# Kernel tuning notes

Hardware: AMD Instinct MI355X
Metric: run time of the kernel (lower is better)

## Reference

```python
import jax, jax.numpy as jnp
import numpy as np

ALPHA = 0.2          # LeakyReLU negative slope
NEG_INF = -9e15      # mask value used by the torch module


def setup_inputs() -> dict:
    key = jax.random.key(0)
    k1, k2, k3, k4 = jax.random.split(key, 4)
    N, F_IN, F_OUT = 8192, 128, 128
    h = jax.random.normal(k1, (N, F_IN), dtype=jnp.float32)
    adj = jax.random.randint(k2, (N, N), 0, 2, dtype=jnp.int32)
    # xavier_uniform(gain=1.414) approximated with scaled normal init
    W = jax.random.normal(k3, (F_IN, F_OUT), dtype=jnp.float32) * (1.414 / np.sqrt(F_IN))
    a = jax.random.normal(k4, (2 * F_OUT, 1), dtype=jnp.float32) * (1.414 / np.sqrt(2 * F_OUT))
    return {"h": h, "adj": adj, "W": W, "a": a}


def reference(h, adj, W, a):
    # Wh: [N, F]
    Wh = h @ W
    F_out = W.shape[1]
    # e[i,j] = LeakyReLU( [Wh_i || Wh_j] . a ) = LeakyReLU( Wh_i.a1 + Wh_j.a2 )
    e_src = Wh @ a[:F_out, 0]   # [N]
    e_dst = Wh @ a[F_out:, 0]   # [N]
    e = jax.nn.leaky_relu(e_src[:, None] + e_dst[None, :], negative_slope=ALPHA)  # [N, N]
    attention = jax.nn.softmax(jnp.where(adj > 0, e, NEG_INF), axis=1)
    # dropout is identity in eval mode
    h_prime = attention @ Wh    # [N, F]
    return h_prime
```

## Files before the change

kernel.cpp:

```cpp
#include <hip/hip_runtime.h>
#include <hip/hip_bf16.h>


#define NN 8192
#define FF 128

typedef __bf16 bf16x8 __attribute__((ext_vector_type(8)));
typedef float floatx4 __attribute__((ext_vector_type(4)));

__device__ __forceinline__ unsigned short f2b(float f) {
    unsigned int u = __float_as_uint(f);
    return (unsigned short)((u + 0x7FFFu + ((u >> 16) & 1u)) >> 16);
}

__global__ __launch_bounds__(128) void k0_uv(const float* __restrict__ W,
                                             const float* __restrict__ a,
                                             float* __restrict__ u,
                                             float* __restrict__ v) {
    int k = blockIdx.x, t = threadIdx.x;
    float wv = W[k * FF + t];
    float p1 = wv * a[t];
    float p2 = wv * a[FF + t];
    for (int off = 32; off; off >>= 1) {
        p1 += __shfl_down(p1, off);
        p2 += __shfl_down(p2, off);
    }
    __shared__ float r[4];
    if ((t & 63) == 0) { r[(t >> 6) * 2] = p1; r[(t >> 6) * 2 + 1] = p2; }
    __syncthreads();
    if (t == 0) { u[k] = r[0] + r[2]; v[k] = r[1] + r[3]; }
}

__global__ __launch_bounds__(256) void k1_wh(const float* __restrict__ h,
                                             const float* __restrict__ W,
                                             const float* __restrict__ u,
                                             const float* __restrict__ v,
                                             unsigned short* __restrict__ WhT,
                                             float* __restrict__ e_src,
                                             float* __restrict__ e_dst) {
    __shared__ float hL[32 * 132];
    __shared__ float wL[128 * 132];
    __shared__ float uL[128], vL[128];
    __shared__ unsigned short tL[128 * 40];

    int t = threadIdx.x;
    int i0 = blockIdx.x * 32;

    {
        int row = t >> 3, c = (t & 7) * 16;
        const float4* s = (const float4*)&h[(i0 + row) * FF + c];
        float4* d = (float4*)&hL[row * 132 + c];
        #pragma unroll
        for (int j = 0; j < 4; j++) d[j] = s[j];
    }
    {
        int row = t >> 1, c = (t & 1) * 64;
        const float4* s = (const float4*)&W[row * FF + c];
        float4* d = (float4*)&wL[row * 132 + c];
        #pragma unroll
        for (int j = 0; j < 16; j++) d[j] = s[j];
    }
    if (t < 128) { uL[t] = u[t]; vL[t] = v[t]; }
    __syncthreads();

    int r0 = (t & 7) * 4;
    int c0 = (t >> 3) * 4;
    float acc[4][4] = {};
    for (int k0 = 0; k0 < 128; k0 += 4) {
        float4 hr[4], wr[4];
        #pragma unroll
        for (int i = 0; i < 4; i++) hr[i] = *(const float4*)&hL[(r0 + i) * 132 + k0];
        #pragma unroll
        for (int i = 0; i < 4; i++) wr[i] = *(const float4*)&wL[(k0 + i) * 132 + c0];
        #pragma unroll
        for (int kj = 0; kj < 4; kj++) {
            const float* hv0 = (const float*)&hr[0];
            #pragma unroll
            for (int ri = 0; ri < 4; ri++) {
                float hvv = ((const float*)&hr[ri])[kj];
                const float* wvv = (const float*)&wr[kj];
                #pragma unroll
                for (int cj = 0; cj < 4; cj++) acc[ri][cj] = fmaf(hvv, wvv[cj], acc[ri][cj]);
            }
            (void)hv0;
        }
    }
    #pragma unroll
    for (int ri = 0; ri < 4; ri++)
        #pragma unroll
        for (int cj = 0; cj < 4; cj++)
            tL[(c0 + cj) * 40 + r0 + ri] = f2b(acc[ri][cj]);
    __syncthreads();

    if (t < 64) {
        int row = t & 31;
        const float* sv = (t < 32) ? uL : vL;
        float s = 0.f;
        for (int k = 0; k < 128; k += 4) {
            float4 h4 = *(const float4*)&hL[row * 132 + k];
            float4 s4 = *(const float4*)&sv[k];
            s = fmaf(h4.x, s4.x, s); s = fmaf(h4.y, s4.y, s);
            s = fmaf(h4.z, s4.z, s); s = fmaf(h4.w, s4.w, s);
        }
        (t < 32 ? e_src : e_dst)[i0 + row] = s;
    }
    {
        int f = t & 127, half = t >> 7;
        const uint4* s = (const uint4*)&tL[f * 40 + half * 16];
        uint4* d = (uint4*)&WhT[f * NN + i0 + half * 16];
        d[0] = s[0]; d[1] = s[1];
    }
}

__device__ __forceinline__ float mask_w(int a, float x) {
    float l = fmaxf(x, 0.2f * x);
    return a > 0 ? __expf(l) : 0.f;
}

__global__ __launch_bounds__(512) void k2_gat(const int* __restrict__ adj,
                                              const unsigned short* __restrict__ WhT,
                                              const float* __restrict__ e_src,
                                              const float* __restrict__ e_dst,
                                              float* __restrict__ out) {
    __shared__ unsigned short wt[32 * 72];
    __shared__ float esL[32];
    __shared__ float dpart[32 * 16];
    __shared__ float denomL[32];

    int t = threadIdx.x;
    int i0 = blockIdx.x * 32;
    if (t < 32) esL[t] = e_src[i0 + t];

    int ii = t & 31;
    int q  = t >> 5;
    int jj0 = q * 4;
    int lane = t & 63, wave = t >> 6;
    int mrow = lane & 15, quad = lane >> 4;
    int n0 = wave * 16;

    const unsigned short* Bbase = WhT + (size_t)(n0 + mrow) * NN + quad * 8;
    const int* Abase = adj + (size_t)(i0 + ii) * NN + jj0;

    floatx4 acc0 = {0.f, 0.f, 0.f, 0.f};
    floatx4 acc1 = {0.f, 0.f, 0.f, 0.f};
    float dsum = 0.f;
    __syncthreads();
    float es_i = esL[ii];

    for (int j0 = 0; j0 < NN; j0 += 64) {
        int4 av = *(const int4*)(Abase + j0);
        float4 ed = *(const float4*)&e_dst[j0 + jj0];
        bf16x8 b0 = *(const bf16x8*)(Bbase + j0);
        bf16x8 b1 = *(const bf16x8*)(Bbase + j0 + 32);

        float w0 = mask_w(av.x, es_i + ed.x);
        float w1 = mask_w(av.y, es_i + ed.y);
        float w2 = mask_w(av.z, es_i + ed.z);
        float w3 = mask_w(av.w, es_i + ed.w);
        dsum += (w0 + w1) + (w2 + w3);
        ushort4 wp = make_ushort4(f2b(w0), f2b(w1), f2b(w2), f2b(w3));

        __syncthreads();
        *(ushort4*)&wt[ii * 72 + jj0] = wp;
        __syncthreads();

        bf16x8 a00 = *(const bf16x8*)&wt[mrow * 72 + quad * 8];
        bf16x8 a10 = *(const bf16x8*)&wt[(16 + mrow) * 72 + quad * 8];
        bf16x8 a01 = *(const bf16x8*)&wt[mrow * 72 + 32 + quad * 8];
        bf16x8 a11 = *(const bf16x8*)&wt[(16 + mrow) * 72 + 32 + quad * 8];

        acc0 = __builtin_amdgcn_mfma_f32_16x16x32_bf16(a00, b0, acc0, 0, 0, 0);
        acc1 = __builtin_amdgcn_mfma_f32_16x16x32_bf16(a10, b0, acc1, 0, 0, 0);
        acc0 = __builtin_amdgcn_mfma_f32_16x16x32_bf16(a01, b1, acc0, 0, 0, 0);
        acc1 = __builtin_amdgcn_mfma_f32_16x16x32_bf16(a11, b1, acc1, 0, 0, 0);
    }

    dpart[ii * 16 + q] = dsum;
    __syncthreads();
    if (t < 32) {
        float s = 0.f;
        #pragma unroll
        for (int k = 0; k < 16; k++) s += dpart[t * 16 + k];
        denomL[t] = 1.0f / s;
    }
    __syncthreads();

    #pragma unroll
    for (int r = 0; r < 4; r++) {
        int row0 = quad * 4 + r;
        out[(i0 + row0) * FF + n0 + mrow] = acc0[r] * denomL[row0];
        int row1 = 16 + row0;
        out[(i0 + row1) * FF + n0 + mrow] = acc1[r] * denomL[row1];
    }
}

extern "C" void kernel_launch(void* const* d_in, const int* in_sizes, int n_in,
                              void* d_out, int out_size, void* d_ws, size_t ws_size,
                              hipStream_t stream) {
    const float* h   = (const float*)d_in[0];
    const int*   adj = (const int*)d_in[1];
    const float* W   = (const float*)d_in[2];
    const float* a   = (const float*)d_in[3];
    float* out = (float*)d_out;

    char* ws = (char*)d_ws;
    unsigned short* WhT = (unsigned short*)ws;
    float* u     = (float*)(ws + 2097152);
    float* v     = u + 128;
    float* e_src = v + 128;
    float* e_dst = e_src + NN;

    k0_uv<<<dim3(128), dim3(128), 0, stream>>>(W, a, u, v);
    k1_wh<<<dim3(256), dim3(256), 0, stream>>>(h, W, u, v, WhT, e_src, e_dst);
    k2_gat<<<dim3(256), dim3(512), 0, stream>>>(adj, WhT, e_src, e_dst, out);
}
```

Baseline: 492.6 us.

## Split GAT reduction over column segments with atomics, double-buffered LDS and swizzle

Splits the N-long column reduction of the attention kernel into four segments so the grid grows from 256 to 1024 blocks, and combines the partial numerators and denominators with float atomics followed by a separate normalization kernel. The main loop is software-pipelined: global loads for the next tile are issued before the MFMAs on the current tile, and the LDS weight tile is double-buffered so only one barrier per iteration remains. The LDS layout is XOR-swizzled to avoid bank conflicts. The cost is two memsets, an extra kernel launch, atomic traffic on the output, and nondeterministic summation order.

New measurement: 419.3 us. 1.17x faster.

```diff
diff --git a/kernel.cpp b/kernel.cpp
--- a/kernel.cpp
+++ b/kernel.cpp
@@ -4,6 +4,9 @@
 
 #define NN 8192
 #define FF 128
+#define SEG 4
+#define JSEG (NN / SEG)
+#define ITERS (JSEG / 64)
 
 typedef __bf16 bf16x8 __attribute__((ext_vector_type(8)));
 typedef float floatx4 __attribute__((ext_vector_type(4)));
@@ -74,7 +77,6 @@
         for (int i = 0; i < 4; i++) wr[i] = *(const float4*)&wL[(k0 + i) * 132 + c0];
         #pragma unroll
         for (int kj = 0; kj < 4; kj++) {
-            const float* hv0 = (const float*)&hr[0];
             #pragma unroll
             for (int ri = 0; ri < 4; ri++) {
                 float hvv = ((const float*)&hr[ri])[kj];
@@ -82,7 +84,6 @@
                 #pragma unroll
                 for (int cj = 0; cj < 4; cj++) acc[ri][cj] = fmaf(hvv, wvv[cj], acc[ri][cj]);
             }
-            (void)hv0;
         }
     }
     #pragma unroll
@@ -117,29 +118,39 @@
     return a > 0 ? __expf(l) : 0.f;
 }
 
-__global__ __launch_bounds__(512) void k2_gat(const int* __restrict__ adj,
-                                              const unsigned short* __restrict__ WhT,
-                                              const float* __restrict__ e_src,
-                                              const float* __restrict__ e_dst,
-                                              float* __restrict__ out) {
-    __shared__ unsigned short wt[32 * 72];
+__global__ __launch_bounds__(512, 4) void k2_gat(const int* __restrict__ adj,
+                                                 const unsigned short* __restrict__ WhT,
+                                                 const float* __restrict__ e_src,
+                                                 const float* __restrict__ e_dst,
+                                                 float* __restrict__ num,
+                                                 float* __restrict__ den) {
+    __shared__ unsigned short wt[2][32 * 64];
     __shared__ float esL[32];
-    __shared__ float dpart[32 * 16];
-    __shared__ float denomL[32];
+    __shared__ float dpart[32 * 17];
 
     int t = threadIdx.x;
-    int i0 = blockIdx.x * 32;
+    int bx = blockIdx.x;
+    int g = bx >> 2, seg = bx & 3;
+    int i0 = g * 32;
+    int jbase = seg * JSEG;
+
     if (t < 32) esL[t] = e_src[i0 + t];
 
     int ii = t & 31;
     int q  = t >> 5;
-    int jj0 = q * 4;
     int lane = t & 63, wave = t >> 6;
     int mrow = lane & 15, quad = lane >> 4;
     int n0 = wave * 16;
 
-    const unsigned short* Bbase = WhT + (size_t)(n0 + mrow) * NN + quad * 8;
-    const int* Abase = adj + (size_t)(i0 + ii) * NN + jj0;
+    const unsigned short* Bb = WhT + (size_t)(n0 + mrow) * NN + jbase + quad * 8;
+    const int*   Ab = adj + (size_t)(i0 + ii) * NN + jbase + q * 4;
+    const float* Eb = e_dst + jbase + q * 4;
+
+    int waddr = ii * 64 + (((q >> 1) ^ (ii & 7)) << 3) + ((q & 1) << 2);
+    int ra00 = mrow * 64 + ((quad ^ (mrow & 7)) << 3);
+    int ra01 = mrow * 64 + (((4 + quad) ^ (mrow & 7)) << 3);
+    int ra10 = (16 + mrow) * 64 + ((quad ^ (mrow & 7)) << 3);
+    int ra11 = (16 + mrow) * 64 + (((4 + quad) ^ (mrow & 7)) << 3);
 
     floatx4 acc0 = {0.f, 0.f, 0.f, 0.f};
     floatx4 acc1 = {0.f, 0.f, 0.f, 0.f};
@@ -147,51 +158,85 @@
     __syncthreads();
     float es_i = esL[ii];
 
-    for (int j0 = 0; j0 < NN; j0 += 64) {
-        int4 av = *(const int4*)(Abase + j0);
-        float4 ed = *(const float4*)&e_dst[j0 + jj0];
-        bf16x8 b0 = *(const bf16x8*)(Bbase + j0);
-        bf16x8 b1 = *(const bf16x8*)(Bbase + j0 + 32);
-
+    int4   av = *(const int4*)Ab;
+    float4 ed = *(const float4*)Eb;
+    bf16x8 b0 = *(const bf16x8*)Bb;
+    bf16x8 b1 = *(const bf16x8*)(Bb + 32);
+    {
         float w0 = mask_w(av.x, es_i + ed.x);
         float w1 = mask_w(av.y, es_i + ed.y);
         float w2 = mask_w(av.z, es_i + ed.z);
         float w3 = mask_w(av.w, es_i + ed.w);
         dsum += (w0 + w1) + (w2 + w3);
-        ushort4 wp = make_ushort4(f2b(w0), f2b(w1), f2b(w2), f2b(w3));
-
-        __syncthreads();
-        *(ushort4*)&wt[ii * 72 + jj0] = wp;
-        __syncthreads();
-
-        bf16x8 a00 = *(const bf16x8*)&wt[mrow * 72 + quad * 8];
-        bf16x8 a10 = *(const bf16x8*)&wt[(16 + mrow) * 72 + quad * 8];
-        bf16x8 a01 = *(const bf16x8*)&wt[mrow * 72 + 32 + quad * 8];
-        bf16x8 a11 = *(const bf16x8*)&wt[(16 + mrow) * 72 + 32 + quad * 8];
-
+        *(ushort4*)&wt[0][waddr] = make_ushort4(f2b(w0), f2b(w1), f2b(w2), f2b(w3));
+    }
+    __syncthreads();
+
+    for (int k = 0; k < ITERS - 1; k++) {
+        int joff = (k + 1) * 64;
+        int4   av2 = *(const int4*)(Ab + joff);
+        float4 ed2 = *(const float4*)(Eb + joff);
+        bf16x8 nb0 = *(const bf16x8*)(Bb + joff);
+        bf16x8 nb1 = *(const bf16x8*)(Bb + joff + 32);
+
+        const unsigned short* buf = wt[k & 1];
+        bf16x8 a00 = *(const bf16x8*)&buf[ra00];
+        bf16x8 a10 = *(const bf16x8*)&buf[ra10];
+        bf16x8 a01 = *(const bf16x8*)&buf[ra01];
+        bf16x8 a11 = *(const bf16x8*)&buf[ra11];
         acc0 = __builtin_amdgcn_mfma_f32_16x16x32_bf16(a00, b0, acc0, 0, 0, 0);
         acc1 = __builtin_amdgcn_mfma_f32_16x16x32_bf16(a10, b0, acc1, 0, 0, 0);
         acc0 = __builtin_amdgcn_mfma_f32_16x16x32_bf16(a01, b1, acc0, 0, 0, 0);
         acc1 = __builtin_amdgcn_mfma_f32_16x16x32_bf16(a11, b1, acc1, 0, 0, 0);
-    }
-
-    dpart[ii * 16 + q] = dsum;
+
+        float w0 = mask_w(av2.x, es_i + ed2.x);
+        float w1 = mask_w(av2.y, es_i + ed2.y);
+        float w2 = mask_w(av2.z, es_i + ed2.z);
+        float w3 = mask_w(av2.w, es_i + ed2.w);
+        dsum += (w0 + w1) + (w2 + w3);
+        *(ushort4*)&wt[(k + 1) & 1][waddr] = make_ushort4(f2b(w0), f2b(w1), f2b(w2), f2b(w3));
+        b0 = nb0; b1 = nb1;
+        __syncthreads();
+    }
+    {
+        const unsigned short* buf = wt[(ITERS - 1) & 1];
+        bf16x8 a00 = *(const bf16x8*)&buf[ra00];
+        bf16x8 a10 = *(const bf16x8*)&buf[ra10];
+        bf16x8 a01 = *(const bf16x8*)&buf[ra01];
+        bf16x8 a11 = *(const bf16x8*)&buf[ra11];
+        acc0 = __builtin_amdgcn_mfma_f32_16x16x32_bf16(a00, b0, acc0, 0, 0, 0);
+        acc1 = __builtin_amdgcn_mfma_f32_16x16x32_bf16(a10, b0, acc1, 0, 0, 0);
+        acc0 = __builtin_amdgcn_mfma_f32_16x16x32_bf16(a01, b1, acc0, 0, 0, 0);
+        acc1 = __builtin_amdgcn_mfma_f32_16x16x32_bf16(a11, b1, acc1, 0, 0, 0);
+    }
+
+    dpart[ii * 17 + q] = dsum;
     __syncthreads();
     if (t < 32) {
         float s = 0.f;
         #pragma unroll
-        for (int k = 0; k < 16; k++) s += dpart[t * 16 + k];
-        denomL[t] = 1.0f / s;
-    }
-    __syncthreads();
+        for (int k = 0; k < 16; k++) s += dpart[t * 17 + k];
+        atomicAdd(&den[i0 + t], s);
+    }
 
     #pragma unroll
     for (int r = 0; r < 4; r++) {
         int row0 = quad * 4 + r;
-        out[(i0 + row0) * FF + n0 + mrow] = acc0[r] * denomL[row0];
-        int row1 = 16 + row0;
-        out[(i0 + row1) * FF + n0 + mrow] = acc1[r] * denomL[row1];
-    }
+        atomicAdd(&num[(size_t)(i0 + row0) * FF + n0 + mrow], acc0[r]);
+        atomicAdd(&num[(size_t)(i0 + 16 + row0) * FF + n0 + mrow], acc1[r]);
+    }
+}
+
+__global__ __launch_bounds__(256) void k3_scale(float* __restrict__ out,
+                                                const float* __restrict__ den) {
+    int idx = blockIdx.x * 256 + threadIdx.x;
+    int i = idx >> 5;
+    int c = (idx & 31) << 2;
+    float r = 1.0f / den[i];
+    float4* p = (float4*)&out[(size_t)i * FF + c];
+    float4 v = *p;
+    v.x *= r; v.y *= r; v.z *= r; v.w *= r;
+    *p = v;
 }
 
 extern "C" void kernel_launch(void* const* d_in, const int* in_sizes, int n_in,
@@ -209,8 +254,13 @@
     float* v     = u + 128;
     float* e_src = v + 128;
     float* e_dst = e_src + NN;
+    float* den   = e_dst + NN;
+
+    hipMemsetAsync(out, 0, (size_t)NN * FF * sizeof(float), stream);
+    hipMemsetAsync(den, 0, (size_t)NN * sizeof(float), stream);
 
     k0_uv<<<dim3(128), dim3(128), 0, stream>>>(W, a, u, v);
     k1_wh<<<dim3(256), dim3(256), 0, stream>>>(h, W, u, v, WhT, e_src, e_dst);
-    k2_gat<<<dim3(256), dim3(512), 0, stream>>>(adj, WhT, e_src, e_dst, out);
-}
+    k2_gat<<<dim3(256 * SEG), dim3(512), 0, stream>>>(adj, WhT, e_src, e_dst, out, den);
+    k3_scale<<<dim3(NN * FF / 4 / 256), dim3(256), 0, stream>>>(out, den);
+}
```

## Split GAT aggregation over key segments with larger row tiles and merge pass

Applied to the files above, without the earlier changes.

Restructures the attention-aggregation kernel so each block handles 128 rows over one eighth of the key dimension, with 8 waves tiling a 128x128 output and reusing each WhT fragment across more rows. It adds a double-buffered, XOR-swizzled LDS tile for the bf16 attention weights, prefetches the next adjacency chunk, and drops to one barrier per step. Partial numerators and denominators go to workspace and a new merge kernel sums and normalizes them. This raises parallelism (512 blocks instead of 256) and cuts redundant WhT reads, at the cost of a 32MB partial-sum round trip and an extra launch.

Result: faster. 425.4 us (-13.6%).

```diff
diff --git a/kernel.cpp b/kernel.cpp
--- a/kernel.cpp
+++ b/kernel.cpp
@@ -4,6 +4,10 @@
 
 #define NN 8192
 #define FF 128
+#define SEGS 8
+#define KSEG (NN / SEGS)
+#define KC 64
+#define NCH (KSEG / KC)
 
 typedef __bf16 bf16x8 __attribute__((ext_vector_type(8)));
 typedef float floatx4 __attribute__((ext_vector_type(4)));
@@ -11,6 +15,9 @@
 __device__ __forceinline__ unsigned short f2b(float f) {
     unsigned int u = __float_as_uint(f);
     return (unsigned short)((u + 0x7FFFu + ((u >> 16) & 1u)) >> 16);
+}
+__device__ __forceinline__ unsigned int pk2(float a, float b) {
+    return (unsigned int)f2b(a) | ((unsigned int)f2b(b) << 16);
 }
 
 __global__ __launch_bounds__(128) void k0_uv(const float* __restrict__ W,
@@ -74,7 +81,6 @@
         for (int i = 0; i < 4; i++) wr[i] = *(const float4*)&wL[(k0 + i) * 132 + c0];
         #pragma unroll
         for (int kj = 0; kj < 4; kj++) {
-            const float* hv0 = (const float*)&hr[0];
             #pragma unroll
             for (int ri = 0; ri < 4; ri++) {
                 float hvv = ((const float*)&hr[ri])[kj];
@@ -82,7 +88,6 @@
                 #pragma unroll
                 for (int cj = 0; cj < 4; cj++) acc[ri][cj] = fmaf(hvv, wvv[cj], acc[ri][cj]);
             }
-            (void)hv0;
         }
     }
     #pragma unroll
@@ -117,81 +122,155 @@
     return a > 0 ? __expf(l) : 0.f;
 }
 
-__global__ __launch_bounds__(512) void k2_gat(const int* __restrict__ adj,
-                                              const unsigned short* __restrict__ WhT,
-                                              const float* __restrict__ e_src,
-                                              const float* __restrict__ e_dst,
-                                              float* __restrict__ out) {
-    __shared__ unsigned short wt[32 * 72];
-    __shared__ float esL[32];
-    __shared__ float dpart[32 * 16];
-    __shared__ float denomL[32];
+__global__ __launch_bounds__(512, 4) void k2_gat(const int* __restrict__ adj,
+                                                 const unsigned short* __restrict__ WhT,
+                                                 const float* __restrict__ e_src,
+                                                 const float* __restrict__ e_dst,
+                                                 float* __restrict__ num_ws,
+                                                 float* __restrict__ den_ws) {
+    __shared__ unsigned short Pt[2][128 * 64];
 
     int t = threadIdx.x;
-    int i0 = blockIdx.x * 32;
-    if (t < 32) esL[t] = e_src[i0 + t];
-
-    int ii = t & 31;
-    int q  = t >> 5;
-    int jj0 = q * 4;
+    int bx = blockIdx.x;
+    int ib = bx >> 3, seg = bx & 7;
+    int i0 = ib * 128;
+    int jb = seg * KSEG;
+
+    int pr = t >> 2;
+    int pc = (t & 3) * 16;
+    int r7 = pr & 7;
+    int g0 = (t & 3) * 2;
+    float es = e_src[i0 + pr];
+    const int*   Ab = adj + (size_t)(i0 + pr) * NN + jb + pc;
+    const float* Eb = e_dst + jb + pc;
+    int wlo = pr * 64 + (((g0 + 0) ^ r7) << 3);
+    int whi = pr * 64 + (((g0 + 1) ^ r7) << 3);
+
     int lane = t & 63, wave = t >> 6;
+    int mg = wave & 3, ng = wave >> 2;
     int mrow = lane & 15, quad = lane >> 4;
-    int n0 = wave * 16;
-
-    const unsigned short* Bbase = WhT + (size_t)(n0 + mrow) * NN + quad * 8;
-    const int* Abase = adj + (size_t)(i0 + ii) * NN + jj0;
-
-    floatx4 acc0 = {0.f, 0.f, 0.f, 0.f};
-    floatx4 acc1 = {0.f, 0.f, 0.f, 0.f};
+
+    const unsigned short* Bp[4];
+    #pragma unroll
+    for (int bn = 0; bn < 4; bn++)
+        Bp[bn] = WhT + (size_t)(ng * 64 + bn * 16 + mrow) * NN + jb + quad * 8;
+
+    int arow[2];
+    arow[0] = mg * 32 + mrow;
+    arow[1] = mg * 32 + 16 + mrow;
+    int aoff[2][2];
+    #pragma unroll
+    for (int a = 0; a < 2; a++)
+        #pragma unroll
+        for (int ks = 0; ks < 2; ks++)
+            aoff[a][ks] = arow[a] * 64 + (((ks * 4 + quad) ^ (arow[a] & 7)) << 3);
+
+    floatx4 acc[2][4] = {};
     float dsum = 0.f;
-    __syncthreads();
-    float es_i = esL[ii];
-
-    for (int j0 = 0; j0 < NN; j0 += 64) {
-        int4 av = *(const int4*)(Abase + j0);
-        float4 ed = *(const float4*)&e_dst[j0 + jj0];
-        bf16x8 b0 = *(const bf16x8*)(Bbase + j0);
-        bf16x8 b1 = *(const bf16x8*)(Bbase + j0 + 32);
-
-        float w0 = mask_w(av.x, es_i + ed.x);
-        float w1 = mask_w(av.y, es_i + ed.y);
-        float w2 = mask_w(av.z, es_i + ed.z);
-        float w3 = mask_w(av.w, es_i + ed.w);
-        dsum += (w0 + w1) + (w2 + w3);
-        ushort4 wp = make_ushort4(f2b(w0), f2b(w1), f2b(w2), f2b(w3));
+
+    int4 av[4];
+    #pragma unroll
+    for (int j = 0; j < 4; j++) av[j] = *(const int4*)(Ab + 4 * j);
+
+    for (int ch = 0; ch < NCH; ch++) {
+        unsigned short* buf = Pt[ch & 1];
+        float4 ev0 = *(const float4*)(Eb + ch * KC);
+        float4 ev1 = *(const float4*)(Eb + ch * KC + 4);
+        float4 ev2 = *(const float4*)(Eb + ch * KC + 8);
+        float4 ev3 = *(const float4*)(Eb + ch * KC + 12);
+        float w[16];
+        w[0]  = mask_w(av[0].x, es + ev0.x);
+        w[1]  = mask_w(av[0].y, es + ev0.y);
+        w[2]  = mask_w(av[0].z, es + ev0.z);
+        w[3]  = mask_w(av[0].w, es + ev0.w);
+        w[4]  = mask_w(av[1].x, es + ev1.x);
+        w[5]  = mask_w(av[1].y, es + ev1.y);
+        w[6]  = mask_w(av[1].z, es + ev1.z);
+        w[7]  = mask_w(av[1].w, es + ev1.w);
+        w[8]  = mask_w(av[2].x, es + ev2.x);
+        w[9]  = mask_w(av[2].y, es + ev2.y);
+        w[10] = mask_w(av[2].z, es + ev2.z);
+        w[11] = mask_w(av[2].w, es + ev2.w);
+        w[12] = mask_w(av[3].x, es + ev3.x);
+        w[13] = mask_w(av[3].y, es + ev3.y);
+        w[14] = mask_w(av[3].z, es + ev3.z);
+        w[15] = mask_w(av[3].w, es + ev3.w);
+        #pragma unroll
+        for (int j = 0; j < 16; j++) dsum += w[j];
+        uint4 lo = make_uint4(pk2(w[0], w[1]), pk2(w[2], w[3]),
+                              pk2(w[4], w[5]), pk2(w[6], w[7]));
+        uint4 hi = make_uint4(pk2(w[8], w[9]), pk2(w[10], w[11]),
+                              pk2(w[12], w[13]), pk2(w[14], w[15]));
+        *(uint4*)&buf[wlo] = lo;
+        *(uint4*)&buf[whi] = hi;
+
+        int nxt = (ch + 1 < NCH) ? (ch + 1) * KC : 0;
+        #pragma unroll
+        for (int j = 0; j < 4; j++) av[j] = *(const int4*)(Ab + nxt + 4 * j);
+
+        bf16x8 b0[4];
+        #pragma unroll
+        for (int bn = 0; bn < 4; bn++) b0[bn] = *(const bf16x8*)(Bp[bn] + ch * KC);
 
         __syncthreads();
-        *(ushort4*)&wt[ii * 72 + jj0] = wp;
-        __syncthreads();
-
-        bf16x8 a00 = *(const bf16x8*)&wt[mrow * 72 + quad * 8];
-        bf16x8 a10 = *(const bf16x8*)&wt[(16 + mrow) * 72 + quad * 8];
-        bf16x8 a01 = *(const bf16x8*)&wt[mrow * 72 + 32 + quad * 8];
-        bf16x8 a11 = *(const bf16x8*)&wt[(16 + mrow) * 72 + 32 + quad * 8];
-
-        acc0 = __builtin_amdgcn_mfma_f32_16x16x32_bf16(a00, b0, acc0, 0, 0, 0);
-        acc1 = __builtin_amdgcn_mfma_f32_16x16x32_bf16(a10, b0, acc1, 0, 0, 0);
-        acc0 = __builtin_amdgcn_mfma_f32_16x16x32_bf16(a01, b1, acc0, 0, 0, 0);
-        acc1 = __builtin_amdgcn_mfma_f32_16x16x32_bf16(a11, b1, acc1, 0, 0, 0);
-    }
-
-    dpart[ii * 16 + q] = dsum;
-    __syncthreads();
-    if (t < 32) {
-        float s = 0.f;
-        #pragma unroll
-        for (int k = 0; k < 16; k++) s += dpart[t * 16 + k];
-        denomL[t] = 1.0f / s;
-    }
-    __syncthreads();
-
-    #pragma unroll
-    for (int r = 0; r < 4; r++) {
-        int row0 = quad * 4 + r;
-        out[(i0 + row0) * FF + n0 + mrow] = acc0[r] * denomL[row0];
-        int row1 = 16 + row0;
-        out[(i0 + row1) * FF + n0 + mrow] = acc1[r] * denomL[row1];
-    }
+
+        const unsigned short* rbuf = Pt[ch & 1];
+        bf16x8 A0[2], A1[2];
+        #pragma unroll
+        for (int a = 0; a < 2; a++) A0[a] = *(const bf16x8*)&rbuf[aoff[a][0]];
+        #pragma unroll
+        for (int a = 0; a < 2; a++) A1[a] = *(const bf16x8*)&rbuf[aoff[a][1]];
+
+        bf16x8 b1[4];
+        #pragma unroll
+        for (int bn = 0; bn < 4; bn++) b1[bn] = *(const bf16x8*)(Bp[bn] + ch * KC + 32);
+
+        #pragma unroll
+        for (int a = 0; a < 2; a++)
+            #pragma unroll
+            for (int bn = 0; bn < 4; bn++)
+                acc[a][bn] = __builtin_amdgcn_mfma_f32_16x16x32_bf16(A0[a], b0[bn], acc[a][bn], 0, 0, 0);
+        #pragma unroll
+        for (int a = 0; a < 2; a++)
+            #pragma unroll
+            for (int bn = 0; bn < 4; bn++)
+                acc[a][bn] = __builtin_amdgcn_mfma_f32_16x16x32_bf16(A1[a], b1[bn], acc[a][bn], 0, 0, 0);
+    }
+
+    dsum += __shfl_xor(dsum, 1);
+    dsum += __shfl_xor(dsum, 2);
+    if ((t & 3) == 0) den_ws[seg * NN + i0 + pr] = dsum;
+
+    float* np = num_ws + (size_t)seg * NN * FF;
+    #pragma unroll
+    for (int a = 0; a < 2; a++)
+        #pragma unroll
+        for (int bn = 0; bn < 4; bn++)
+            #pragma unroll
+            for (int r = 0; r < 4; r++) {
+                int row = mg * 32 + a * 16 + quad * 4 + r;
+                int col = ng * 64 + bn * 16 + mrow;
+                np[(size_t)(i0 + row) * FF + col] = acc[a][bn][r];
+            }
+}
+
+__global__ __launch_bounds__(256) void k3_merge(const float* __restrict__ num_ws,
+                                                const float* __restrict__ den_ws,
+                                                float* __restrict__ out) {
+    int idx = blockIdx.x * 256 + threadIdx.x;
+    int i = idx >> 5;
+    int c = (idx & 31) << 2;
+    float4 s = make_float4(0.f, 0.f, 0.f, 0.f);
+    float d = 0.f;
+    #pragma unroll
+    for (int sg = 0; sg < SEGS; sg++) {
+        float4 vv = *(const float4*)&num_ws[(size_t)sg * NN * FF + (size_t)i * FF + c];
+        s.x += vv.x; s.y += vv.y; s.z += vv.z; s.w += vv.w;
+        d += den_ws[sg * NN + i];
+    }
+    float r = 1.0f / d;
+    s.x *= r; s.y *= r; s.z *= r; s.w *= r;
+    *(float4*)&out[(size_t)i * FF + c] = s;
 }
 
 extern "C" void kernel_launch(void* const* d_in, const int* in_sizes, int n_in,
@@ -207,10 +286,13 @@
     unsigned short* WhT = (unsigned short*)ws;
     float* u     = (float*)(ws + 2097152);
     float* v     = u + 128;
-    float* e_src = v + 128;
+    float* e_src = (float*)(ws + 2097152 + 1024);
     float* e_dst = e_src + NN;
+    float* num_ws = (float*)(ws + 4194304);
+    float* den_ws = (float*)(ws + 4194304 + 33554432);
 
     k0_uv<<<dim3(128), dim3(128), 0, stream>>>(W, a, u, v);
     k1_wh<<<dim3(256), dim3(256), 0, stream>>>(h, W, u, v, WhT, e_src, e_dst);
-    k2_gat<<<dim3(256), dim3(512), 0, stream>>>(adj, WhT, e_src, e_dst, out);
-}
+    k2_gat<<<dim3((NN / 128) * SEGS), dim3(512), 0, stream>>>(adj, WhT, e_src, e_dst, num_ws, den_ws);
+    k3_merge<<<dim3(NN * FF / 4 / 256), dim3(256), 0, stream>>>(num_ws, den_ws, out);
+}
```

## Split GAT aggregation over column segments with register-resident attention weights and merge pass

Applied to the files above, without the earlier changes.

The attention-aggregation kernel now gives each block 128 rows and one of 8 column segments, producing partial numerators and denominators that a new merge kernel sums and normalises. Each lane computes its own bf16 attention weights directly in MFMA A-operand layout, which removes the shared-memory round trip and the two barriers per iteration, and it prefetches the next adj and e_dst chunk. Each wave covers all 128 output features with 8 accumulators, so the WhT B-operand is reused across 16 rows instead of being refetched by many narrow blocks. In exchange it writes and rereads a 32 MB partial-sum workspace and adds an extra launch.

New measurement: 483.2 us. About the same (-1.9%).

```diff
diff --git a/kernel.cpp b/kernel.cpp
--- a/kernel.cpp
+++ b/kernel.cpp
@@ -4,6 +4,9 @@
 
 #define NN 8192
 #define FF 128
+#define SEGS 8
+#define JSEG (NN / SEGS)
+#define NK (JSEG / 32)
 
 typedef __bf16 bf16x8 __attribute__((ext_vector_type(8)));
 typedef float floatx4 __attribute__((ext_vector_type(4)));
@@ -11,6 +14,9 @@
 __device__ __forceinline__ unsigned short f2b(float f) {
     unsigned int u = __float_as_uint(f);
     return (unsigned short)((u + 0x7FFFu + ((u >> 16) & 1u)) >> 16);
+}
+__device__ __forceinline__ unsigned int pk2(float a, float b) {
+    return (unsigned int)f2b(a) | ((unsigned int)f2b(b) << 16);
 }
 
 __global__ __launch_bounds__(128) void k0_uv(const float* __restrict__ W,
@@ -74,7 +80,6 @@
         for (int i = 0; i < 4; i++) wr[i] = *(const float4*)&wL[(k0 + i) * 132 + c0];
         #pragma unroll
         for (int kj = 0; kj < 4; kj++) {
-            const float* hv0 = (const float*)&hr[0];
             #pragma unroll
             for (int ri = 0; ri < 4; ri++) {
                 float hvv = ((const float*)&hr[ri])[kj];
@@ -82,7 +87,6 @@
                 #pragma unroll
                 for (int cj = 0; cj < 4; cj++) acc[ri][cj] = fmaf(hvv, wvv[cj], acc[ri][cj]);
             }
-            (void)hv0;
         }
     }
     #pragma unroll
@@ -117,81 +121,106 @@
     return a > 0 ? __expf(l) : 0.f;
 }
 
-__global__ __launch_bounds__(512) void k2_gat(const int* __restrict__ adj,
-                                              const unsigned short* __restrict__ WhT,
-                                              const float* __restrict__ e_src,
-                                              const float* __restrict__ e_dst,
-                                              float* __restrict__ out) {
-    __shared__ unsigned short wt[32 * 72];
-    __shared__ float esL[32];
-    __shared__ float dpart[32 * 16];
-    __shared__ float denomL[32];
-
+__global__ __launch_bounds__(512, 4) void k2_gat(const int* __restrict__ adj,
+                                                 const unsigned short* __restrict__ WhT,
+                                                 const float* __restrict__ e_src,
+                                                 const float* __restrict__ e_dst,
+                                                 float* __restrict__ num_ws,
+                                                 float* __restrict__ den_ws) {
     int t = threadIdx.x;
-    int i0 = blockIdx.x * 32;
-    if (t < 32) esL[t] = e_src[i0 + t];
-
-    int ii = t & 31;
-    int q  = t >> 5;
-    int jj0 = q * 4;
+    int bx = blockIdx.x;
+    int it = bx >> 3, seg = bx & 7;
+    int i0 = it * 128;
+    int jb = seg * JSEG;
+
     int lane = t & 63, wave = t >> 6;
     int mrow = lane & 15, quad = lane >> 4;
-    int n0 = wave * 16;
-
-    const unsigned short* Bbase = WhT + (size_t)(n0 + mrow) * NN + quad * 8;
-    const int* Abase = adj + (size_t)(i0 + ii) * NN + jj0;
-
-    floatx4 acc0 = {0.f, 0.f, 0.f, 0.f};
-    floatx4 acc1 = {0.f, 0.f, 0.f, 0.f};
+    int irow = i0 + wave * 16 + mrow;
+
+    float es = e_src[irow];
+    const int*   Ap = adj + (size_t)irow * NN + jb + quad * 8;
+    const float* Ep = e_dst + jb + quad * 8;
+
+    const unsigned short* Bp[8];
+    #pragma unroll
+    for (int bn = 0; bn < 8; bn++)
+        Bp[bn] = WhT + (size_t)(bn * 16 + mrow) * NN + jb + quad * 8;
+
+    floatx4 acc[8] = {};
     float dsum = 0.f;
-    __syncthreads();
-    float es_i = esL[ii];
-
-    for (int j0 = 0; j0 < NN; j0 += 64) {
-        int4 av = *(const int4*)(Abase + j0);
-        float4 ed = *(const float4*)&e_dst[j0 + jj0];
-        bf16x8 b0 = *(const bf16x8*)(Bbase + j0);
-        bf16x8 b1 = *(const bf16x8*)(Bbase + j0 + 32);
-
-        float w0 = mask_w(av.x, es_i + ed.x);
-        float w1 = mask_w(av.y, es_i + ed.y);
-        float w2 = mask_w(av.z, es_i + ed.z);
-        float w3 = mask_w(av.w, es_i + ed.w);
-        dsum += (w0 + w1) + (w2 + w3);
-        ushort4 wp = make_ushort4(f2b(w0), f2b(w1), f2b(w2), f2b(w3));
-
-        __syncthreads();
-        *(ushort4*)&wt[ii * 72 + jj0] = wp;
-        __syncthreads();
-
-        bf16x8 a00 = *(const bf16x8*)&wt[mrow * 72 + quad * 8];
-        bf16x8 a10 = *(const bf16x8*)&wt[(16 + mrow) * 72 + quad * 8];
-        bf16x8 a01 = *(const bf16x8*)&wt[mrow * 72 + 32 + quad * 8];
-        bf16x8 a11 = *(const bf16x8*)&wt[(16 + mrow) * 72 + 32 + quad * 8];
-
-        acc0 = __builtin_amdgcn_mfma_f32_16x16x32_bf16(a00, b0, acc0, 0, 0, 0);
-        acc1 = __builtin_amdgcn_mfma_f32_16x16x32_bf16(a10, b0, acc1, 0, 0, 0);
-        acc0 = __builtin_amdgcn_mfma_f32_16x16x32_bf16(a01, b1, acc0, 0, 0, 0);
-        acc1 = __builtin_amdgcn_mfma_f32_16x16x32_bf16(a11, b1, acc1, 0, 0, 0);
-    }
-
-    dpart[ii * 16 + q] = dsum;
-    __syncthreads();
-    if (t < 32) {
-        float s = 0.f;
-        #pragma unroll
-        for (int k = 0; k < 16; k++) s += dpart[t * 16 + k];
-        denomL[t] = 1.0f / s;
-    }
-    __syncthreads();
-
-    #pragma unroll
-    for (int r = 0; r < 4; r++) {
-        int row0 = quad * 4 + r;
-        out[(i0 + row0) * FF + n0 + mrow] = acc0[r] * denomL[row0];
-        int row1 = 16 + row0;
-        out[(i0 + row1) * FF + n0 + mrow] = acc1[r] * denomL[row1];
-    }
+
+    int4   a0 = *(const int4*)Ap;
+    int4   a1 = *(const int4*)(Ap + 4);
+    float4 e0 = *(const float4*)Ep;
+    float4 e1 = *(const float4*)(Ep + 4);
+
+    for (int ks = 0; ks < NK; ks++) {
+        bf16x8 B[8];
+        #pragma unroll
+        for (int bn = 0; bn < 8; bn++)
+            B[bn] = *(const bf16x8*)(Bp[bn] + ks * 32);
+
+        int nxt = (ks + 1 < NK ? ks + 1 : ks) * 32;
+        int4   na0 = *(const int4*)(Ap + nxt);
+        int4   na1 = *(const int4*)(Ap + nxt + 4);
+        float4 ne0 = *(const float4*)(Ep + nxt);
+        float4 ne1 = *(const float4*)(Ep + nxt + 4);
+
+        float w0 = mask_w(a0.x, es + e0.x);
+        float w1 = mask_w(a0.y, es + e0.y);
+        float w2 = mask_w(a0.z, es + e0.z);
+        float w3 = mask_w(a0.w, es + e0.w);
+        float w4 = mask_w(a1.x, es + e1.x);
+        float w5 = mask_w(a1.y, es + e1.y);
+        float w6 = mask_w(a1.z, es + e1.z);
+        float w7 = mask_w(a1.w, es + e1.w);
+        dsum += ((w0 + w1) + (w2 + w3)) + ((w4 + w5) + (w6 + w7));
+
+        union { unsigned int u[4]; bf16x8 v; } af;
+        af.u[0] = pk2(w0, w1);
+        af.u[1] = pk2(w2, w3);
+        af.u[2] = pk2(w4, w5);
+        af.u[3] = pk2(w6, w7);
+        bf16x8 A = af.v;
+
+        #pragma unroll
+        for (int bn = 0; bn < 8; bn++)
+            acc[bn] = __builtin_amdgcn_mfma_f32_16x16x32_bf16(A, B[bn], acc[bn], 0, 0, 0);
+
+        a0 = na0; a1 = na1; e0 = ne0; e1 = ne1;
+    }
+
+    dsum += __shfl_xor(dsum, 16);
+    dsum += __shfl_xor(dsum, 32);
+    if (quad == 0) den_ws[seg * NN + irow] = dsum;
+
+    float* np = num_ws + (size_t)seg * NN * FF;
+    #pragma unroll
+    for (int bn = 0; bn < 8; bn++)
+        #pragma unroll
+        for (int r = 0; r < 4; r++) {
+            int row = i0 + wave * 16 + quad * 4 + r;
+            np[(size_t)row * FF + bn * 16 + mrow] = acc[bn][r];
+        }
+}
+
+__global__ __launch_bounds__(256) void k3_merge(const float* __restrict__ num_ws,
+                                                const float* __restrict__ den_ws,
+                                                float* __restrict__ out) {
+    int idx = blockIdx.x * 256 + threadIdx.x;
+    int i = idx >> 5;
+    int c = (idx & 31) << 2;
+    float4 s = make_float4(0.f, 0.f, 0.f, 0.f);
+    float d = 0.f;
+    #pragma unroll
+    for (int sg = 0; sg < SEGS; sg++) {
+        float4 vv = *(const float4*)&num_ws[(size_t)sg * NN * FF + (size_t)i * FF + c];
+        s.x += vv.x; s.y += vv.y; s.z += vv.z; s.w += vv.w;
+        d += den_ws[sg * NN + i];
+    }
+    float r = 1.0f / d;
+    s.x *= r; s.y *= r; s.z *= r; s.w *= r;
+    *(float4*)&out[(size_t)i * FF + c] = s;
 }
 
 extern "C" void kernel_launch(void* const* d_in, const int* in_sizes, int n_in,
@@ -207,10 +236,13 @@
     unsigned short* WhT = (unsigned short*)ws;
     float* u     = (float*)(ws + 2097152);
     float* v     = u + 128;
-    float* e_src = v + 128;
+    float* e_src = (float*)(ws + 2097152 + 1024);
     float* e_dst = e_src + NN;
+    float* num_ws = (float*)(ws + 4194304);
+    float* den_ws = (float*)(ws + 4194304 + 33554432);
 
     k0_uv<<<dim3(128), dim3(128), 0, stream>>>(W, a, u, v);
     k1_wh<<<dim3(256), dim3(256), 0, stream>>>(h, W, u, v, WhT, e_src, e_dst);
-    k2_gat<<<dim3(256), dim3(512), 0, stream>>>(adj, WhT, e_src, e_dst, out);
-}
+    k2_gat<<<dim3((NN / 128) * SEGS), dim3(512), 0, stream>>>(adj, WhT, e_src, e_dst, num_ws, den_ws);
+    k3_merge<<<dim3(NN * FF / 4 / 256), dim3(256), 0, stream>>>(num_ws, den_ws, out);
+}
```
